# Performance work log

Measured on AMD Instinct MI355X. Metric: run time of the kernel, lower is better.

Reference implementation:

```python
import jax, jax.numpy as jnp
import numpy as np

B, T, J, D = 64, 2048, 128, 512


def setup_inputs() -> dict:
    key = jax.random.key(0)
    k1, k2, k3, k4 = jax.random.split(key, 4)
    question = jax.random.normal(k1, (B, J, D), dtype=jnp.float32)
    context = jax.random.normal(k2, (B, T, D), dtype=jnp.float32)
    question_len = jax.random.randint(k3, (B,), 1, J + 1, dtype=jnp.int32)
    context_len = jax.random.randint(k4, (B,), 1, T + 1, dtype=jnp.int32)
    weight = jnp.ones((D, 1), dtype=jnp.float32)  # initializer='ones'
    return {"question": question, "context": context,
            "question_len": question_len, "context_len": context_len,
            "weight": weight}


def reference(question, context, question_len, context_len, weight):
    # Original computes sum_d context[b,t,d]*question[b,j,d]*w[d] via a
    # broadcast [B,T,J,D] intermediate; reformulated as a batched GEMM.
    w = weight[:, 0]                                   # [D]
    sim = jnp.einsum('btd,bjd->btj', context * w, question)  # [B,T,J]
    Jm = question.shape[1]
    Tm = context.shape[1]
    q_mask = (jnp.arange(Jm) < question_len[:, None]).astype(jnp.float32)  # [B,J]
    c_mask = (jnp.arange(Tm) < context_len[:, None]).astype(jnp.float32)   # [B,T]
    mask = c_mask[:, :, None] * q_mask[:, None, :]     # [B,T,J]
    neg = jnp.finfo(jnp.float32).min
    sim = sim + neg * (1.0 - mask)
    attn = jax.nn.softmax(sim, axis=1)                 # softmax over context axis T
    return jnp.sum(attn * mask, axis=2)[..., None]     # [B,T,1]
```

## Files before the change

kernel.cpp:

```cpp
#include <hip/hip_runtime.h>
#include <math.h>

#define BB 64
#define TT 2048
#define JJ 128
#define DD 512
#define BK 32

typedef short short8 __attribute__((ext_vector_type(8)));
typedef float f32x4 __attribute__((ext_vector_type(4)));

__device__ inline unsigned pk_hi(float a, float b) {
  return __builtin_amdgcn_perm(__float_as_uint(b), __float_as_uint(a), 0x07060302u);
}
__device__ inline float truncbf(float x) {
  return __uint_as_float(__float_as_uint(x) & 0xFFFF0000u);
}
__device__ inline void pack8(float4 a, float4 b, uint4& h, uint4& l) {
  h = make_uint4(pk_hi(a.x, a.y), pk_hi(a.z, a.w), pk_hi(b.x, b.y), pk_hi(b.z, b.w));
  float l0 = a.x - truncbf(a.x), l1 = a.y - truncbf(a.y);
  float l2 = a.z - truncbf(a.z), l3 = a.w - truncbf(a.w);
  float l4 = b.x - truncbf(b.x), l5 = b.y - truncbf(b.y);
  float l6 = b.z - truncbf(b.z), l7 = b.w - truncbf(b.w);
  l = make_uint4(pk_hi(l0, l1), pk_hi(l2, l3), pk_hi(l4, l5), pk_hi(l6, l7));
}
__device__ inline short8 bc8(uint4 u) { return __builtin_bit_cast(short8, u); }

__global__ __launch_bounds__(256, 3)
void sim_gemm_mfma(const float* __restrict__ Qm, const float* __restrict__ Cm,
                   const float* __restrict__ w, float* __restrict__ S) {
  __shared__ uint4 Ahi[128 * 4];
  __shared__ uint4 Alo[128 * 4];
  __shared__ uint4 Bhi[128 * 4];
  __shared__ uint4 Blo[128 * 4];

  const int tid = threadIdx.x;
  const int b = blockIdx.y;
  const int t0 = blockIdx.x * 128;

  const int sr = tid >> 1;
  const int sc0 = (tid & 1) * 2;
  const int ssw = (sr >> 1) & 3;
  const int slotA0 = sr * 4 + (sc0 ^ ssw);
  const int slotA1 = sr * 4 + ((sc0 + 1) ^ ssw);

  const float* qp = Qm + ((size_t)b * JJ + sr) * DD + sc0 * 8;
  const float* cp = Cm + ((size_t)b * TT + t0 + sr) * DD + sc0 * 8;
  const float* wp = w + sc0 * 8;

  const int lane = tid & 63;
  const int wv = tid >> 6;
  const int wm = (wv & 1) * 64;
  const int wn = (wv >> 1) * 64;
  const int l15 = lane & 15;
  const int q = lane >> 4;
  const int fchunk = q ^ ((l15 >> 1) & 3);

  int aslot[4], bslot[4];
#pragma unroll
  for (int i = 0; i < 4; i++) {
    aslot[i] = (wm + i * 16 + l15) * 4 + fchunk;
    bslot[i] = (wn + i * 16 + l15) * 4 + fchunk;
  }

  f32x4 acc[4][4] = {};

  for (int ks = 0; ks < 16; ks++) {
    const int k0 = ks * BK;
    float4 q0 = *(const float4*)(qp + k0 + 0);
    float4 q1 = *(const float4*)(qp + k0 + 4);
    float4 q2 = *(const float4*)(qp + k0 + 8);
    float4 q3 = *(const float4*)(qp + k0 + 12);
    float4 w0 = *(const float4*)(wp + k0 + 0);
    float4 w1 = *(const float4*)(wp + k0 + 4);
    float4 w2 = *(const float4*)(wp + k0 + 8);
    float4 w3 = *(const float4*)(wp + k0 + 12);
    float4 c0 = *(const float4*)(cp + k0 + 0);
    float4 c1 = *(const float4*)(cp + k0 + 4);
    float4 c2 = *(const float4*)(cp + k0 + 8);
    float4 c3 = *(const float4*)(cp + k0 + 12);
    q0.x *= w0.x; q0.y *= w0.y; q0.z *= w0.z; q0.w *= w0.w;
    q1.x *= w1.x; q1.y *= w1.y; q1.z *= w1.z; q1.w *= w1.w;
    q2.x *= w2.x; q2.y *= w2.y; q2.z *= w2.z; q2.w *= w2.w;
    q3.x *= w3.x; q3.y *= w3.y; q3.z *= w3.z; q3.w *= w3.w;

    __syncthreads();
    uint4 h, l;
    pack8(q0, q1, h, l); Ahi[slotA0] = h; Alo[slotA0] = l;
    pack8(q2, q3, h, l); Ahi[slotA1] = h; Alo[slotA1] = l;
    pack8(c0, c1, h, l); Bhi[slotA0] = h; Blo[slotA0] = l;
    pack8(c2, c3, h, l); Bhi[slotA1] = h; Blo[slotA1] = l;
    __syncthreads();

    short8 bh[4], bl[4];
#pragma unroll
    for (int ni = 0; ni < 4; ni++) {
      bh[ni] = bc8(Bhi[bslot[ni]]);
      bl[ni] = bc8(Blo[bslot[ni]]);
    }
#pragma unroll
    for (int mi = 0; mi < 4; mi++) {
      short8 ah = bc8(Ahi[aslot[mi]]);
      short8 al = bc8(Alo[aslot[mi]]);
#pragma unroll
      for (int ni = 0; ni < 4; ni++) {
        acc[mi][ni] = __builtin_amdgcn_mfma_f32_16x16x32_bf16(ah, bh[ni], acc[mi][ni], 0, 0, 0);
        acc[mi][ni] = __builtin_amdgcn_mfma_f32_16x16x32_bf16(al, bh[ni], acc[mi][ni], 0, 0, 0);
        acc[mi][ni] = __builtin_amdgcn_mfma_f32_16x16x32_bf16(ah, bl[ni], acc[mi][ni], 0, 0, 0);
      }
    }
  }

#pragma unroll
  for (int mi = 0; mi < 4; mi++) {
#pragma unroll
    for (int ni = 0; ni < 4; ni++) {
      const int j = wm + mi * 16 + q * 4;
      const int t = t0 + wn + ni * 16 + l15;
      float* dst = S + ((size_t)b * JJ + j) * TT + t;
      dst[0 * TT] = acc[mi][ni][0];
      dst[1 * TT] = acc[mi][ni][1];
      dst[2 * TT] = acc[mi][ni][2];
      dst[3 * TT] = acc[mi][ni][3];
    }
  }
}

__global__ __launch_bounds__(256)
void softmax_stats_kernel(const float* __restrict__ S, const int* __restrict__ qlen,
                          const int* __restrict__ clen, float* __restrict__ m_out,
                          float* __restrict__ r_out) {
  const int j = blockIdx.x;
  const int b = blockIdx.y;
  if (j >= qlen[b]) return;
  const int cl = clen[b];
  const int tid = threadIdx.x;
  const float4* row = (const float4*)(S + ((size_t)b * JJ + j) * TT);

  float4 v0 = row[tid];
  float4 v1 = row[tid + 256];
  const int t0 = tid * 4;
  const int t1 = (tid + 256) * 4;
  const float NEG = -3.4e38f;

  float m = NEG;
  m = fmaxf(m, (t0 + 0 < cl) ? v0.x : NEG);
  m = fmaxf(m, (t0 + 1 < cl) ? v0.y : NEG);
  m = fmaxf(m, (t0 + 2 < cl) ? v0.z : NEG);
  m = fmaxf(m, (t0 + 3 < cl) ? v0.w : NEG);
  m = fmaxf(m, (t1 + 0 < cl) ? v1.x : NEG);
  m = fmaxf(m, (t1 + 1 < cl) ? v1.y : NEG);
  m = fmaxf(m, (t1 + 2 < cl) ? v1.z : NEG);
  m = fmaxf(m, (t1 + 3 < cl) ? v1.w : NEG);

  __shared__ float red[8];
#pragma unroll
  for (int off = 32; off > 0; off >>= 1) m = fmaxf(m, __shfl_down(m, off));
  if ((tid & 63) == 0) red[tid >> 6] = m;
  __syncthreads();
  m = fmaxf(fmaxf(red[0], red[1]), fmaxf(red[2], red[3]));

  float s = 0.f;
  s += (t0 + 0 < cl) ? __expf(v0.x - m) : 0.f;
  s += (t0 + 1 < cl) ? __expf(v0.y - m) : 0.f;
  s += (t0 + 2 < cl) ? __expf(v0.z - m) : 0.f;
  s += (t0 + 3 < cl) ? __expf(v0.w - m) : 0.f;
  s += (t1 + 0 < cl) ? __expf(v1.x - m) : 0.f;
  s += (t1 + 1 < cl) ? __expf(v1.y - m) : 0.f;
  s += (t1 + 2 < cl) ? __expf(v1.z - m) : 0.f;
  s += (t1 + 3 < cl) ? __expf(v1.w - m) : 0.f;
#pragma unroll
  for (int off = 32; off > 0; off >>= 1) s += __shfl_down(s, off);
  if ((tid & 63) == 0) red[4 + (tid >> 6)] = s;
  __syncthreads();
  s = red[4] + red[5] + red[6] + red[7];

  if (tid == 0) {
    m_out[(size_t)b * JJ + j] = m;
    r_out[(size_t)b * JJ + j] = 1.f / s;
  }
}

__global__ __launch_bounds__(256)
void out_kernel(const float* __restrict__ S, const float* __restrict__ m_arr,
                const float* __restrict__ r_arr, const int* __restrict__ qlen,
                const int* __restrict__ clen, float* __restrict__ out) {
  const int b = blockIdx.y;
  const int t = blockIdx.x * 256 + threadIdx.x;
  const int ql = qlen[b];
  const int cl = clen[b];

  __shared__ float lm[JJ];
  __shared__ float lr[JJ];
  if (threadIdx.x < ql) {
    lm[threadIdx.x] = m_arr[(size_t)b * JJ + threadIdx.x];
    lr[threadIdx.x] = r_arr[(size_t)b * JJ + threadIdx.x];
  }
  __syncthreads();

  float acc = 0.f;
  if (t < cl) {
    const float* col = S + (size_t)b * JJ * TT + t;
#pragma unroll 4
    for (int j = 0; j < ql; j++) {
      acc += __expf(col[(size_t)j * TT] - lm[j]) * lr[j];
    }
  }
  out[(size_t)b * TT + t] = acc;
}

extern "C" void kernel_launch(void* const* d_in, const int* in_sizes, int n_in,
                              void* d_out, int out_size, void* d_ws, size_t ws_size,
                              hipStream_t stream) {
  const float* question = (const float*)d_in[0];
  const float* context  = (const float*)d_in[1];
  const int*   qlen     = (const int*)d_in[2];
  const int*   clen     = (const int*)d_in[3];
  const float* weight   = (const float*)d_in[4];
  float* out = (float*)d_out;

  float* S = (float*)d_ws;
  float* m_arr = S + (size_t)BB * JJ * TT;
  float* r_arr = m_arr + (size_t)BB * JJ;

  sim_gemm_mfma<<<dim3(TT / 128, BB), 256, 0, stream>>>(question, context, weight, S);
  softmax_stats_kernel<<<dim3(JJ, BB), 256, 0, stream>>>(S, qlen, clen, m_arr, r_arr);
  out_kernel<<<dim3(TT / 256, BB), 256, 0, stream>>>(S, m_arr, r_arr, qlen, clen, out);
}
```

Measured before the change: 446.1 us.

## Prepack weighted question to bf16 hi/lo and DMA tiles directly into LDS

Adds a prepass kernel that multiplies the question by the weight and splits it into swizzled bf16 hi/lo tiles in workspace, so the GEMM no longer repeats that packing for every context tile. The GEMM now loads Q and C tiles into LDS with global_load_lds DMA instead of going through registers, and splits the context into hi/lo after reading it back from LDS. It also remaps block IDs so neighbouring blocks land on different batches. The cost is an extra launch, extra workspace traffic for the packed Q, and larger raw fp32 C tiles held in LDS.

```diff
diff --git a/kernel.cpp b/kernel.cpp
--- a/kernel.cpp
+++ b/kernel.cpp
@@ -1,4 +1,5 @@
 #include <hip/hip_runtime.h>
+#include <stdint.h>
 #include <math.h>
 
 #define BB 64
@@ -9,6 +10,13 @@
 
 typedef short short8 __attribute__((ext_vector_type(8)));
 typedef float f32x4 __attribute__((ext_vector_type(4)));
+
+typedef const __attribute__((address_space(1))) uint32_t glb_u32;
+typedef __attribute__((address_space(3))) uint32_t lds_u32;
+
+__device__ __forceinline__ void dma16(const void* g, void* l) {
+  __builtin_amdgcn_global_load_lds((glb_u32*)g, (lds_u32*)l, 16, 0, 0);
+}
 
 __device__ inline unsigned pk_hi(float a, float b) {
   return __builtin_amdgcn_perm(__float_as_uint(b), __float_as_uint(a), 0x07060302u);
@@ -26,82 +34,96 @@
 }
 __device__ inline short8 bc8(uint4 u) { return __builtin_bit_cast(short8, u); }
 
+__global__ __launch_bounds__(256)
+void qpack_kernel(const float* __restrict__ Qm, const float* __restrict__ w,
+                  uint4* __restrict__ Qhi, uint4* __restrict__ Qlo) {
+  const int gid = blockIdx.x * 256 + threadIdx.x;
+  const int c = gid & 3;
+  const int ks = (gid >> 2) & 15;
+  const int j = (gid >> 6) & 127;
+  const int b = gid >> 13;
+  const float* qp = Qm + (((size_t)b * JJ + j) * DD) + ks * BK + c * 8;
+  const float* wp = w + ks * BK + c * 8;
+  float4 a = *(const float4*)qp;
+  float4 bq = *(const float4*)(qp + 4);
+  float4 wa = *(const float4*)wp;
+  float4 wb = *(const float4*)(wp + 4);
+  a.x *= wa.x; a.y *= wa.y; a.z *= wa.z; a.w *= wa.w;
+  bq.x *= wb.x; bq.y *= wb.y; bq.z *= wb.z; bq.w *= wb.w;
+  uint4 h, l;
+  pack8(a, bq, h, l);
+  const int slot = j * 4 + (c ^ ((j >> 1) & 3));
+  const size_t o = ((size_t)(b * 16 + ks)) * 512 + slot;
+  Qhi[o] = h;
+  Qlo[o] = l;
+}
+
 __global__ __launch_bounds__(256, 3)
-void sim_gemm_mfma(const float* __restrict__ Qm, const float* __restrict__ Cm,
-                   const float* __restrict__ w, float* __restrict__ S) {
-  __shared__ uint4 Ahi[128 * 4];
-  __shared__ uint4 Alo[128 * 4];
-  __shared__ uint4 Bhi[128 * 4];
-  __shared__ uint4 Blo[128 * 4];
+void sim_gemm_mfma(const uint4* __restrict__ Qhi, const uint4* __restrict__ Qlo,
+                   const float* __restrict__ Cm, float* __restrict__ S) {
+  __shared__ uint4 Ah[512];
+  __shared__ uint4 Al[512];
+  __shared__ uint4 Cl[1024];
 
   const int tid = threadIdx.x;
-  const int b = blockIdx.y;
-  const int t0 = blockIdx.x * 128;
-
-  const int sr = tid >> 1;
-  const int sc0 = (tid & 1) * 2;
-  const int ssw = (sr >> 1) & 3;
-  const int slotA0 = sr * 4 + (sc0 ^ ssw);
-  const int slotA1 = sr * 4 + ((sc0 + 1) ^ ssw);
-
-  const float* qp = Qm + ((size_t)b * JJ + sr) * DD + sc0 * 8;
-  const float* cp = Cm + ((size_t)b * TT + t0 + sr) * DD + sc0 * 8;
-  const float* wp = w + sc0 * 8;
-
   const int lane = tid & 63;
   const int wv = tid >> 6;
+
+  const int id = blockIdx.x;
+  const int nid = (id & 7) * 128 + (id >> 3);
+  const int b = nid >> 4;
+  const int t0 = (nid & 15) * 128;
+
+  const uint4* qh_src = Qhi + (size_t)b * 8192 + wv * 128 + lane;
+  const uint4* ql_src = Qlo + (size_t)b * 8192 + wv * 128 + lane;
+  char* ah_dst = (char*)Ah + wv * 2048;
+  char* al_dst = (char*)Al + wv * 2048;
+  const int crow = wv * 32 + (lane >> 3);
+  const int cch = (lane & 7) ^ ((lane >> 3) & 7);
+  const float* c_src = Cm + ((size_t)b * TT + t0 + crow) * DD + cch * 4;
+  char* cl_dst = (char*)Cl + wv * 4096;
+
   const int wm = (wv & 1) * 64;
   const int wn = (wv >> 1) * 64;
   const int l15 = lane & 15;
   const int q = lane >> 4;
   const int fchunk = q ^ ((l15 >> 1) & 3);
-
-  int aslot[4], bslot[4];
-#pragma unroll
-  for (int i = 0; i < 4; i++) {
-    aslot[i] = (wm + i * 16 + l15) * 4 + fchunk;
-    bslot[i] = (wn + i * 16 + l15) * 4 + fchunk;
-  }
+  const int swl = l15 & 7;
+
+  int aslot[4];
+#pragma unroll
+  for (int i = 0; i < 4; i++) aslot[i] = (wm + i * 16 + l15) * 4 + fchunk;
 
   f32x4 acc[4][4] = {};
 
   for (int ks = 0; ks < 16; ks++) {
-    const int k0 = ks * BK;
-    float4 q0 = *(const float4*)(qp + k0 + 0);
-    float4 q1 = *(const float4*)(qp + k0 + 4);
-    float4 q2 = *(const float4*)(qp + k0 + 8);
-    float4 q3 = *(const float4*)(qp + k0 + 12);
-    float4 w0 = *(const float4*)(wp + k0 + 0);
-    float4 w1 = *(const float4*)(wp + k0 + 4);
-    float4 w2 = *(const float4*)(wp + k0 + 8);
-    float4 w3 = *(const float4*)(wp + k0 + 12);
-    float4 c0 = *(const float4*)(cp + k0 + 0);
-    float4 c1 = *(const float4*)(cp + k0 + 4);
-    float4 c2 = *(const float4*)(cp + k0 + 8);
-    float4 c3 = *(const float4*)(cp + k0 + 12);
-    q0.x *= w0.x; q0.y *= w0.y; q0.z *= w0.z; q0.w *= w0.w;
-    q1.x *= w1.x; q1.y *= w1.y; q1.z *= w1.z; q1.w *= w1.w;
-    q2.x *= w2.x; q2.y *= w2.y; q2.z *= w2.z; q2.w *= w2.w;
-    q3.x *= w3.x; q3.y *= w3.y; q3.z *= w3.z; q3.w *= w3.w;
-
     __syncthreads();
-    uint4 h, l;
-    pack8(q0, q1, h, l); Ahi[slotA0] = h; Alo[slotA0] = l;
-    pack8(q2, q3, h, l); Ahi[slotA1] = h; Alo[slotA1] = l;
-    pack8(c0, c1, h, l); Bhi[slotA0] = h; Blo[slotA0] = l;
-    pack8(c2, c3, h, l); Bhi[slotA1] = h; Blo[slotA1] = l;
+#pragma unroll
+    for (int s = 0; s < 2; s++) {
+      dma16(qh_src + ks * 512 + s * 64, ah_dst + s * 1024);
+      dma16(ql_src + ks * 512 + s * 64, al_dst + s * 1024);
+    }
+#pragma unroll
+    for (int s = 0; s < 4; s++) {
+      dma16(c_src + (size_t)ks * BK + s * 8 * DD, cl_dst + s * 1024);
+    }
     __syncthreads();
 
     short8 bh[4], bl[4];
 #pragma unroll
     for (int ni = 0; ni < 4; ni++) {
-      bh[ni] = bc8(Bhi[bslot[ni]]);
-      bl[ni] = bc8(Blo[bslot[ni]]);
+      const int row = wn + ni * 16 + l15;
+      float4 v0 = __builtin_bit_cast(float4, Cl[row * 8 + ((2 * q) ^ swl)]);
+      float4 v1 = __builtin_bit_cast(float4, Cl[row * 8 + ((2 * q + 1) ^ swl)]);
+      uint4 h, l;
+      pack8(v0, v1, h, l);
+      bh[ni] = bc8(h);
+      bl[ni] = bc8(l);
     }
 #pragma unroll
     for (int mi = 0; mi < 4; mi++) {
-      short8 ah = bc8(Ahi[aslot[mi]]);
-      short8 al = bc8(Alo[aslot[mi]]);
+      short8 ah = bc8(Ah[aslot[mi]]);
+      short8 al = bc8(Al[aslot[mi]]);
 #pragma unroll
       for (int ni = 0; ni < 4; ni++) {
         acc[mi][ni] = __builtin_amdgcn_mfma_f32_16x16x32_bf16(ah, bh[ni], acc[mi][ni], 0, 0, 0);
@@ -222,8 +244,11 @@
   float* S = (float*)d_ws;
   float* m_arr = S + (size_t)BB * JJ * TT;
   float* r_arr = m_arr + (size_t)BB * JJ;
-
-  sim_gemm_mfma<<<dim3(TT / 128, BB), 256, 0, stream>>>(question, context, weight, S);
+  uint4* Qhi = (uint4*)(r_arr + (size_t)BB * JJ);
+  uint4* Qlo = Qhi + (size_t)BB * 16 * 512;
+
+  qpack_kernel<<<dim3(2048), 256, 0, stream>>>(question, weight, Qhi, Qlo);
+  sim_gemm_mfma<<<dim3(1024), 256, 0, stream>>>(Qhi, Qlo, context, S);
   softmax_stats_kernel<<<dim3(JJ, BB), 256, 0, stream>>>(S, qlen, clen, m_arr, r_arr);
   out_kernel<<<dim3(TT / 256, BB), 256, 0, stream>>>(S, m_arr, r_arr, qlen, clen, out);
 }
```

New measurement: 415.8 us. 1.07x faster.
